# Kernel optimization log

Measured on AMD Instinct MI355X. Metric: run time of the kernel, lower is better.

## Reference

```python
import jax, jax.numpy as jnp
import numpy as np

B, C, H, W, K, O, KS = 32, 16, 256, 256, 4, 16, 3
C4 = C // 4


def setup_inputs() -> dict:
    key = jax.random.key(0)
    ks = jax.random.split(key, 6)
    return {
        "x": jax.random.normal(ks[0], (B, C, H, W), dtype=jnp.float32),
        "weight": jax.random.normal(ks[1], (K, O, C, KS, KS), dtype=jnp.float32),
        "attn_w1": jax.random.normal(ks[2], (C4, C), dtype=jnp.float32) * 0.1,
        "attn_b1": jnp.zeros((C4,), dtype=jnp.float32),
        "attn_w2": jax.random.normal(ks[3], (K, C4), dtype=jnp.float32) * 0.1,
        "attn_b2": jnp.zeros((K,), dtype=jnp.float32),
    }


def reference(x, weight, attn_w1, attn_b1, attn_w2, attn_b2):
    # Attention branch: global avg pool -> 1x1 conv -> relu -> 1x1 conv -> softmax over K
    pooled = x.mean(axis=(2, 3))                                  # (B, C)
    h = jax.nn.relu(pooled @ attn_w1.T + attn_b1)                 # (B, C//4)
    attn = jax.nn.softmax(h @ attn_w2.T + attn_b2, axis=1)        # (B, K)

    # Per-sample aggregated kernel: sum_k attn[b,k] * weight[k]
    agg_w = jnp.einsum('bk,koihw->boihw', attn, weight)           # (B, O, C, KS, KS)

    # Per-sample conv2d (equivalent to torch grouped conv with groups=B)
    pad = ((1, 1), (1, 1))
    def per_sample(xi, wi):
        # xi: (C, H, W), wi: (O, C, KS, KS)
        return jax.lax.conv_general_dilated(
            xi[None], wi, window_strides=(1, 1), padding=pad,
            dimension_numbers=('NCHW', 'OIHW', 'NCHW'))[0]
    return jax.vmap(per_sample)(x, agg_w)                         # (B, O, H, W)
```

## Files before the change

kernel.cpp:

```cpp
#include <hip/hip_runtime.h>

#define BD  32
#define CD  16
#define HD  256
#define WD  256
#define KD  4
#define OD  16
#define C4D 4

typedef __attribute__((ext_vector_type(8))) short short8v;
typedef __attribute__((ext_vector_type(4))) float float4v;

__device__ float          g_partial[2048];
__device__ unsigned short g_wfrag[BD * 2 * 5 * 64 * 8];

__device__ __forceinline__ unsigned short bf16_rne(float f) {
    unsigned u = __builtin_bit_cast(unsigned, f);
    u += 0x7FFFu + ((u >> 16) & 1u);
    return (unsigned short)(u >> 16);
}
__device__ __forceinline__ float bf16_to_f(unsigned short h) {
    unsigned u = ((unsigned)h) << 16;
    return __builtin_bit_cast(float, u);
}

__global__ void pool_kernel(const float* __restrict__ x) {
    const int plane = blockIdx.x >> 2;
    const int part  = blockIdx.x & 3;
    const float4* xp4 = reinterpret_cast<const float4*>(
        x + (size_t)plane * (HD * WD) + part * (HD * WD / 4));

    float4 v[16];
    #pragma unroll
    for (int i = 0; i < 16; ++i) v[i] = xp4[threadIdx.x + i * 256];
    float s = 0.f;
    #pragma unroll
    for (int i = 0; i < 16; ++i) s += (v[i].x + v[i].y) + (v[i].z + v[i].w);

    __shared__ float red[256];
    red[threadIdx.x] = s;
    __syncthreads();
    for (int off = 128; off > 0; off >>= 1) {
        if (threadIdx.x < off) red[threadIdx.x] += red[threadIdx.x + off];
        __syncthreads();
    }
    if (threadIdx.x == 0) g_partial[blockIdx.x] = red[0];
}

__global__ void attn_agg_kernel(const float* __restrict__ w1, const float* __restrict__ b1,
                                const float* __restrict__ w2, const float* __restrict__ b2,
                                const float* __restrict__ weight) {
    const int b = blockIdx.x;

    float p[CD];
    #pragma unroll
    for (int c = 0; c < CD; ++c) {
        const int i0 = (b * CD + c) * 4;
        p[c] = (g_partial[i0] + g_partial[i0 + 1] + g_partial[i0 + 2] + g_partial[i0 + 3])
               * (1.f / (HD * WD));
    }

    float h[C4D];
    #pragma unroll
    for (int j = 0; j < C4D; ++j) {
        float s = b1[j];
        #pragma unroll
        for (int c = 0; c < CD; ++c) s = fmaf(p[c], w1[j * CD + c], s);
        h[j] = fmaxf(s, 0.f);
    }

    float lg[KD];
    float mx = -1e30f;
    #pragma unroll
    for (int k = 0; k < KD; ++k) {
        float s = b2[k];
        #pragma unroll
        for (int j = 0; j < C4D; ++j) s = fmaf(h[j], w2[k * C4D + j], s);
        lg[k] = s;
        mx = fmaxf(mx, s);
    }
    float se = 0.f;
    #pragma unroll
    for (int k = 0; k < KD; ++k) { lg[k] = expf(lg[k] - mx); se += lg[k]; }
    const float inv = 1.f / se;
    float at[KD];
    #pragma unroll
    for (int k = 0; k < KD; ++k) at[k] = lg[k] * inv;

    for (int e = threadIdx.x; e < 5120; e += 256) {
        const int prod = e / 2560;
        const int rem  = e % 2560;
        const int s    = rem / 512;
        const int lr   = rem % 512;
        const int lane = lr >> 3;
        const int i    = lr & 7;
        const int o    = lane & 15;
        const int kg   = lane >> 4;
        const int kk   = kg * 8 + i;
        const int tl   = kk >> 4;
        const int c    = kk & 15;
        const int tap  = 2 * s + tl;
        float v = 0.f;
        if (tap < 9) {
            #pragma unroll
            for (int k = 0; k < KD; ++k)
                v = fmaf(at[k], weight[((k * OD + o) * CD + c) * 9 + tap], v);
        }
        const unsigned short hi = bf16_rne(v);
        unsigned short val = hi;
        if (prod == 1) val = bf16_rne(v - bf16_to_f(hi));
        g_wfrag[b * 5120 + e] = val;
    }
}

__global__ __launch_bounds__(256, 2)
void conv_kernel(const float* __restrict__ x, float* __restrict__ out) {
    const int b  = blockIdx.y;
    const int tx = blockIdx.x & 3;
    const int ty = blockIdx.x >> 2;
    const int x0 = tx * 64, y0 = ty * 16;

    __shared__ unsigned short xs[18 * 66 * 24];

    for (int e = threadIdx.x; e < 18 * 66; e += 256) {
        const int r   = e / 66;
        const int col = e - r * 66;
        const int gy  = y0 - 1 + r;
        const int gx  = x0 - 1 + col;
        const bool ok = (gy >= 0) && (gy < HD) && (gx >= 0) && (gx < WD);
        const float* px = x + ((size_t)b * CD * HD * WD) + (size_t)gy * WD + gx;
        unsigned d[8];
        #pragma unroll
        for (int j = 0; j < 8; ++j) {
            float v0 = 0.f, v1 = 0.f;
            if (ok) {
                v0 = px[(size_t)(2 * j)     * (HD * WD)];
                v1 = px[(size_t)(2 * j + 1) * (HD * WD)];
            }
            d[j] = (unsigned)bf16_rne(v0) | ((unsigned)bf16_rne(v1) << 16);
        }
        unsigned* dst = reinterpret_cast<unsigned*>(&xs[e * 24]);
        *reinterpret_cast<uint4*>(dst)     = make_uint4(d[0], d[1], d[2], d[3]);
        *reinterpret_cast<uint4*>(dst + 4) = make_uint4(d[4], d[5], d[6], d[7]);
    }

    const int lane = threadIdx.x & 63;
    const int wv   = threadIdx.x >> 6;

    short8v whi[5], wlo[5];
    {
        const unsigned short* wf = g_wfrag + b * 5120;
        #pragma unroll
        for (int s = 0; s < 5; ++s) {
            whi[s] = *(const short8v*)&wf[s * 512 + lane * 8];
            wlo[s] = *(const short8v*)&wf[2560 + s * 512 + lane * 8];
        }
    }

    const int m     = lane & 15;
    const int kg    = lane >> 4;
    const int tl    = kg >> 1;
    const int chalf = kg & 1;
    int aoff[5];
    #pragma unroll
    for (int s = 0; s < 5; ++s) {
        int tap = 2 * s + tl;
        if (tap > 8) tap = 8;
        const int dy = tap / 3 - 1, dx = tap % 3 - 1;
        aoff[s] = (dy * 66 + dx) * 24;
    }
    const int colbase = 1 + 16 * wv + m;

    __syncthreads();

    #pragma unroll 1
    for (int q2 = 0; q2 < 8; ++q2) {
        const int qa = 2 * q2;
        const int pa = ((qa + 1) * 66 + colbase) * 24 + chalf * 8;
        const int pb = pa + 66 * 24;
        float4v acca = {0.f, 0.f, 0.f, 0.f};
        float4v accb = {0.f, 0.f, 0.f, 0.f};
        #pragma unroll
        for (int s = 0; s < 5; ++s) {
            const short8v Aa = *(const short8v*)&xs[pa + aoff[s]];
            const short8v Ab = *(const short8v*)&xs[pb + aoff[s]];
            acca = __builtin_amdgcn_mfma_f32_16x16x32_bf16(Aa, whi[s], acca, 0, 0, 0);
            accb = __builtin_amdgcn_mfma_f32_16x16x32_bf16(Ab, whi[s], accb, 0, 0, 0);
            acca = __builtin_amdgcn_mfma_f32_16x16x32_bf16(Aa, wlo[s], acca, 0, 0, 0);
            accb = __builtin_amdgcn_mfma_f32_16x16x32_bf16(Ab, wlo[s], accb, 0, 0, 0);
        }
        const int o  = lane & 15;
        const int xc = x0 + 16 * wv + kg * 4;
        float4 va = make_float4(acca[0], acca[1], acca[2], acca[3]);
        float4 vb = make_float4(accb[0], accb[1], accb[2], accb[3]);
        *reinterpret_cast<float4*>(
            &out[((size_t)(b * OD + o) * HD + (y0 + qa)) * WD + xc]) = va;
        *reinterpret_cast<float4*>(
            &out[((size_t)(b * OD + o) * HD + (y0 + qa + 1)) * WD + xc]) = vb;
    }
}

extern "C" void kernel_launch(void* const* d_in, const int* in_sizes, int n_in,
                              void* d_out, int out_size, void* d_ws, size_t ws_size,
                              hipStream_t stream) {
    (void)in_sizes; (void)n_in; (void)out_size; (void)d_ws; (void)ws_size;
    const float* x      = (const float*)d_in[0];
    const float* weight = (const float*)d_in[1];
    const float* w1     = (const float*)d_in[2];
    const float* b1     = (const float*)d_in[3];
    const float* w2     = (const float*)d_in[4];
    const float* b2     = (const float*)d_in[5];
    float* out = (float*)d_out;

    pool_kernel<<<2048, 256, 0, stream>>>(x);
    attn_agg_kernel<<<32, 256, 0, stream>>>(w1, b1, w2, b2, weight);
    conv_kernel<<<dim3(64, 32), 256, 0, stream>>>(x, out);
}
```

Baseline: 299.8 us.

## Emit bf16 copy of input during pooling and load it in conv

The pooling pass now also writes a bf16 copy of the whole input to a global scratch buffer. The conv kernel stages its halo tile from that buffer with wide 8-byte row loads plus a small edge-column path, instead of scalar fp32 gathers converted per element. The attention/aggregation kernel is split across four blocks per sample for more parallelism. This adds a 64 MB bf16 write and read in exchange for halving conv input bytes and coalescing the tile load.

```diff
diff --git a/kernel.cpp b/kernel.cpp
--- a/kernel.cpp
+++ b/kernel.cpp
@@ -12,6 +12,7 @@
 typedef __attribute__((ext_vector_type(4))) float float4v;
 
 __device__ float          g_partial[2048];
+__device__ unsigned short g_xbf[(size_t)BD * CD * HD * WD];
 __device__ unsigned short g_wfrag[BD * 2 * 5 * 64 * 8];
 
 __device__ __forceinline__ unsigned short bf16_rne(float f) {
@@ -27,15 +28,22 @@
 __global__ void pool_kernel(const float* __restrict__ x) {
     const int plane = blockIdx.x >> 2;
     const int part  = blockIdx.x & 3;
-    const float4* xp4 = reinterpret_cast<const float4*>(
-        x + (size_t)plane * (HD * WD) + part * (HD * WD / 4));
+    const size_t base = (size_t)plane * (HD * WD) + part * (HD * WD / 4);
+    const float4* xp4 = reinterpret_cast<const float4*>(x + base);
 
     float4 v[16];
     #pragma unroll
     for (int i = 0; i < 16; ++i) v[i] = xp4[threadIdx.x + i * 256];
+
     float s = 0.f;
     #pragma unroll
-    for (int i = 0; i < 16; ++i) s += (v[i].x + v[i].y) + (v[i].z + v[i].w);
+    for (int i = 0; i < 16; ++i) {
+        s += (v[i].x + v[i].y) + (v[i].z + v[i].w);
+        ushort4 h;
+        h.x = bf16_rne(v[i].x); h.y = bf16_rne(v[i].y);
+        h.z = bf16_rne(v[i].z); h.w = bf16_rne(v[i].w);
+        *reinterpret_cast<ushort4*>(&g_xbf[base + (size_t)(threadIdx.x + i * 256) * 4]) = h;
+    }
 
     __shared__ float red[256];
     red[threadIdx.x] = s;
@@ -50,7 +58,8 @@
 __global__ void attn_agg_kernel(const float* __restrict__ w1, const float* __restrict__ b1,
                                 const float* __restrict__ w2, const float* __restrict__ b2,
                                 const float* __restrict__ weight) {
-    const int b = blockIdx.x;
+    const int b  = blockIdx.x >> 2;
+    const int e0 = (blockIdx.x & 3) * 1280;
 
     float p[CD];
     #pragma unroll
@@ -87,7 +96,7 @@
     #pragma unroll
     for (int k = 0; k < KD; ++k) at[k] = lg[k] * inv;
 
-    for (int e = threadIdx.x; e < 5120; e += 256) {
+    for (int e = e0 + threadIdx.x; e < e0 + 1280; e += 256) {
         const int prod = e / 2560;
         const int rem  = e % 2560;
         const int s    = rem / 512;
@@ -114,7 +123,7 @@
 }
 
 __global__ __launch_bounds__(256, 2)
-void conv_kernel(const float* __restrict__ x, float* __restrict__ out) {
+void conv_kernel(float* __restrict__ out) {
     const int b  = blockIdx.y;
     const int tx = blockIdx.x & 3;
     const int ty = blockIdx.x >> 2;
@@ -122,23 +131,53 @@
 
     __shared__ unsigned short xs[18 * 66 * 24];
 
-    for (int e = threadIdx.x; e < 18 * 66; e += 256) {
-        const int r   = e / 66;
-        const int col = e - r * 66;
+    for (int grp = threadIdx.x; grp < 288; grp += 256) {
+        const int r  = grp >> 4;
+        const int j  = grp & 15;
+        const int gy = y0 - 1 + r;
+        const int gx = x0 + 4 * j;
+        const bool ok = (gy >= 0) && (gy < HD);
+        uint2 v[16];
+        #pragma unroll
+        for (int c = 0; c < 16; ++c) {
+            v[c] = make_uint2(0u, 0u);
+            if (ok)
+                v[c] = *reinterpret_cast<const uint2*>(
+                    &g_xbf[((size_t)(b * CD + c) * HD + gy) * WD + gx]);
+        }
+        #pragma unroll
+        for (int p = 0; p < 4; ++p) {
+            unsigned d[8];
+            #pragma unroll
+            for (int i = 0; i < 8; ++i) {
+                const unsigned a0 = (p < 2) ? v[2 * i].x     : v[2 * i].y;
+                const unsigned a1 = (p < 2) ? v[2 * i + 1].x : v[2 * i + 1].y;
+                d[i] = (p & 1) ? ((a0 >> 16) | (a1 & 0xFFFF0000u))
+                               : ((a0 & 0xFFFFu) | (a1 << 16));
+            }
+            const int e = r * 66 + 4 * j + 1 + p;
+            unsigned* dst = reinterpret_cast<unsigned*>(&xs[e * 24]);
+            *reinterpret_cast<uint4*>(dst)     = make_uint4(d[0], d[1], d[2], d[3]);
+            *reinterpret_cast<uint4*>(dst + 4) = make_uint4(d[4], d[5], d[6], d[7]);
+        }
+    }
+    if (threadIdx.x < 36) {
+        const int r   = threadIdx.x >> 1;
+        const int col = (threadIdx.x & 1) ? 65 : 0;
         const int gy  = y0 - 1 + r;
         const int gx  = x0 - 1 + col;
         const bool ok = (gy >= 0) && (gy < HD) && (gx >= 0) && (gx < WD);
-        const float* px = x + ((size_t)b * CD * HD * WD) + (size_t)gy * WD + gx;
         unsigned d[8];
         #pragma unroll
-        for (int j = 0; j < 8; ++j) {
-            float v0 = 0.f, v1 = 0.f;
+        for (int i = 0; i < 8; ++i) {
+            unsigned u0 = 0, u1 = 0;
             if (ok) {
-                v0 = px[(size_t)(2 * j)     * (HD * WD)];
-                v1 = px[(size_t)(2 * j + 1) * (HD * WD)];
+                u0 = g_xbf[((size_t)(b * CD + 2 * i)     * HD + gy) * WD + gx];
+                u1 = g_xbf[((size_t)(b * CD + 2 * i + 1) * HD + gy) * WD + gx];
             }
-            d[j] = (unsigned)bf16_rne(v0) | ((unsigned)bf16_rne(v1) << 16);
-        }
+            d[i] = u0 | (u1 << 16);
+        }
+        const int e = r * 66 + col;
         unsigned* dst = reinterpret_cast<unsigned*>(&xs[e * 24]);
         *reinterpret_cast<uint4*>(dst)     = make_uint4(d[0], d[1], d[2], d[3]);
         *reinterpret_cast<uint4*>(dst + 4) = make_uint4(d[4], d[5], d[6], d[7]);
@@ -213,6 +252,6 @@
     float* out = (float*)d_out;
 
     pool_kernel<<<2048, 256, 0, stream>>>(x);
-    attn_agg_kernel<<<32, 256, 0, stream>>>(w1, b1, w2, b2, weight);
-    conv_kernel<<<dim3(64, 32), 256, 0, stream>>>(x, out);
-}
+    attn_agg_kernel<<<128, 256, 0, stream>>>(w1, b1, w2, b2, weight);
+    conv_kernel<<<dim3(64, 32), 256, 0, stream>>>(out);
+}
```

Result: no change. 297.5 us (-0.8%).

## Pre-convert input to padded bf16 interleaved layout in pool pass, read directly in conv

Applied to the files above, without the earlier changes.

The pooling kernel now also writes a zero-padded, channel-interleaved bf16 copy of x to a global buffer while it sums. The conv kernel then drops its shared-memory staging and fp32-to-bf16 conversion and loads MFMA operands straight from that buffer through the caches. Pooling partials are reorganised per stripe, the weight aggregation is spread over more blocks, and conv occupancy is raised. This trades an extra global write and read of the bf16 copy, plus cache-dependent halo reuse, for removing the LDS fill and a second fp32 pass over x.

```diff
diff --git a/kernel.cpp b/kernel.cpp
--- a/kernel.cpp
+++ b/kernel.cpp
@@ -11,7 +11,8 @@
 typedef __attribute__((ext_vector_type(8))) short short8v;
 typedef __attribute__((ext_vector_type(4))) float float4v;
 
-__device__ float          g_partial[2048];
+__device__ float          g_partial[64 * 16 * 8];
+__device__ unsigned short g_xi[(size_t)64 * 258 * 258 * 8];
 __device__ unsigned short g_wfrag[BD * 2 * 5 * 64 * 8];
 
 __device__ __forceinline__ unsigned short bf16_rne(float f) {
@@ -24,40 +25,69 @@
     return __builtin_bit_cast(float, u);
 }
 
-__global__ void pool_kernel(const float* __restrict__ x) {
-    const int plane = blockIdx.x >> 2;
-    const int part  = blockIdx.x & 3;
-    const float4* xp4 = reinterpret_cast<const float4*>(
-        x + (size_t)plane * (HD * WD) + part * (HD * WD / 4));
-
-    float4 v[16];
-    #pragma unroll
-    for (int i = 0; i < 16; ++i) v[i] = xp4[threadIdx.x + i * 256];
-    float s = 0.f;
-    #pragma unroll
-    for (int i = 0; i < 16; ++i) s += (v[i].x + v[i].y) + (v[i].z + v[i].w);
-
-    __shared__ float red[256];
-    red[threadIdx.x] = s;
+__global__ __launch_bounds__(256)
+void pool_kernel(const float* __restrict__ x) {
+    const int bb     = blockIdx.x >> 4;
+    const int stripe = blockIdx.x & 15;
+    const int b      = bb >> 1;
+    const int chalf  = bb & 1;
+    const int tid    = threadIdx.x;
+
+    float s8[8] = {0.f, 0.f, 0.f, 0.f, 0.f, 0.f, 0.f, 0.f};
+
+    #pragma unroll 2
+    for (int i = 0; i < 16; ++i) {
+        const int y = stripe * 16 + i;
+        const size_t prow = (size_t)y * WD + tid;
+        float f[8];
+        #pragma unroll
+        for (int ci = 0; ci < 8; ++ci) {
+            f[ci] = x[(size_t)(b * CD + chalf * 8 + ci) * (HD * WD) + prow];
+            s8[ci] += f[ci];
+        }
+        const unsigned d0 = (unsigned)bf16_rne(f[0]) | ((unsigned)bf16_rne(f[1]) << 16);
+        const unsigned d1 = (unsigned)bf16_rne(f[2]) | ((unsigned)bf16_rne(f[3]) << 16);
+        const unsigned d2 = (unsigned)bf16_rne(f[4]) | ((unsigned)bf16_rne(f[5]) << 16);
+        const unsigned d3 = (unsigned)bf16_rne(f[6]) | ((unsigned)bf16_rne(f[7]) << 16);
+        *reinterpret_cast<uint4*>(
+            &g_xi[(((size_t)bb * 258 + (y + 1)) * 258 + (tid + 1)) * 8]) =
+            make_uint4(d0, d1, d2, d3);
+    }
+
+    #pragma unroll
+    for (int ci = 0; ci < 8; ++ci) {
+        float v = s8[ci];
+        #pragma unroll
+        for (int off = 32; off > 0; off >>= 1) v += __shfl_down(v, off, 64);
+        s8[ci] = v;
+    }
+    __shared__ float ws[4][8];
+    const int lane = tid & 63, wv = tid >> 6;
+    if (lane == 0) {
+        #pragma unroll
+        for (int ci = 0; ci < 8; ++ci) ws[wv][ci] = s8[ci];
+    }
     __syncthreads();
-    for (int off = 128; off > 0; off >>= 1) {
-        if (threadIdx.x < off) red[threadIdx.x] += red[threadIdx.x + off];
-        __syncthreads();
-    }
-    if (threadIdx.x == 0) g_partial[blockIdx.x] = red[0];
+    if (tid < 8)
+        g_partial[(bb * 16 + stripe) * 8 + tid] =
+            ws[0][tid] + ws[1][tid] + ws[2][tid] + ws[3][tid];
 }
 
 __global__ void attn_agg_kernel(const float* __restrict__ w1, const float* __restrict__ b1,
                                 const float* __restrict__ w2, const float* __restrict__ b2,
                                 const float* __restrict__ weight) {
-    const int b = blockIdx.x;
+    const int b  = blockIdx.x >> 2;
+    const int e0 = (blockIdx.x & 3) * 1280;
 
     float p[CD];
     #pragma unroll
     for (int c = 0; c < CD; ++c) {
-        const int i0 = (b * CD + c) * 4;
-        p[c] = (g_partial[i0] + g_partial[i0 + 1] + g_partial[i0 + 2] + g_partial[i0 + 3])
-               * (1.f / (HD * WD));
+        const int bb = b * 2 + (c >> 3);
+        const int ci = c & 7;
+        float s = 0.f;
+        #pragma unroll
+        for (int st = 0; st < 16; ++st) s += g_partial[(bb * 16 + st) * 8 + ci];
+        p[c] = s * (1.f / (HD * WD));
     }
 
     float h[C4D];
@@ -87,7 +117,7 @@
     #pragma unroll
     for (int k = 0; k < KD; ++k) at[k] = lg[k] * inv;
 
-    for (int e = threadIdx.x; e < 5120; e += 256) {
+    for (int e = e0 + threadIdx.x; e < e0 + 1280; e += 256) {
         const int prod = e / 2560;
         const int rem  = e % 2560;
         const int s    = rem / 512;
@@ -113,37 +143,12 @@
     }
 }
 
-__global__ __launch_bounds__(256, 2)
-void conv_kernel(const float* __restrict__ x, float* __restrict__ out) {
+__global__ __launch_bounds__(256, 4)
+void conv_kernel(float* __restrict__ out) {
     const int b  = blockIdx.y;
     const int tx = blockIdx.x & 3;
     const int ty = blockIdx.x >> 2;
     const int x0 = tx * 64, y0 = ty * 16;
-
-    __shared__ unsigned short xs[18 * 66 * 24];
-
-    for (int e = threadIdx.x; e < 18 * 66; e += 256) {
-        const int r   = e / 66;
-        const int col = e - r * 66;
-        const int gy  = y0 - 1 + r;
-        const int gx  = x0 - 1 + col;
-        const bool ok = (gy >= 0) && (gy < HD) && (gx >= 0) && (gx < WD);
-        const float* px = x + ((size_t)b * CD * HD * WD) + (size_t)gy * WD + gx;
-        unsigned d[8];
-        #pragma unroll
-        for (int j = 0; j < 8; ++j) {
-            float v0 = 0.f, v1 = 0.f;
-            if (ok) {
-                v0 = px[(size_t)(2 * j)     * (HD * WD)];
-                v1 = px[(size_t)(2 * j + 1) * (HD * WD)];
-            }
-            d[j] = (unsigned)bf16_rne(v0) | ((unsigned)bf16_rne(v1) << 16);
-        }
-        unsigned* dst = reinterpret_cast<unsigned*>(&xs[e * 24]);
-        *reinterpret_cast<uint4*>(dst)     = make_uint4(d[0], d[1], d[2], d[3]);
-        *reinterpret_cast<uint4*>(dst + 4) = make_uint4(d[4], d[5], d[6], d[7]);
-    }
-
     const int lane = threadIdx.x & 63;
     const int wv   = threadIdx.x >> 6;
 
@@ -161,42 +166,46 @@
     const int kg    = lane >> 4;
     const int tl    = kg >> 1;
     const int chalf = kg & 1;
+    const int bb    = b * 2 + chalf;
+    const int col   = x0 + wv * 16 + m;
+    const unsigned short* bptr =
+        g_xi + (((size_t)bb * 258 + (y0 + 1)) * 258 + (col + 1)) * 8;
+
     int aoff[5];
     #pragma unroll
     for (int s = 0; s < 5; ++s) {
         int tap = 2 * s + tl;
         if (tap > 8) tap = 8;
         const int dy = tap / 3 - 1, dx = tap % 3 - 1;
-        aoff[s] = (dy * 66 + dx) * 24;
-    }
-    const int colbase = 1 + 16 * wv + m;
-
-    __syncthreads();
+        aoff[s] = (dy * 258 + dx) * 8;
+    }
+
+    const int o  = lane & 15;
+    const int xc = x0 + wv * 16 + kg * 4;
 
     #pragma unroll 1
     for (int q2 = 0; q2 < 8; ++q2) {
         const int qa = 2 * q2;
-        const int pa = ((qa + 1) * 66 + colbase) * 24 + chalf * 8;
-        const int pb = pa + 66 * 24;
+        const unsigned short* pa = bptr + qa * (258 * 8);
+        const unsigned short* pb = pa + 258 * 8;
         float4v acca = {0.f, 0.f, 0.f, 0.f};
         float4v accb = {0.f, 0.f, 0.f, 0.f};
         #pragma unroll
         for (int s = 0; s < 5; ++s) {
-            const short8v Aa = *(const short8v*)&xs[pa + aoff[s]];
-            const short8v Ab = *(const short8v*)&xs[pb + aoff[s]];
+            const short8v Aa = *(const short8v*)(pa + aoff[s]);
+            const short8v Ab = *(const short8v*)(pb + aoff[s]);
             acca = __builtin_amdgcn_mfma_f32_16x16x32_bf16(Aa, whi[s], acca, 0, 0, 0);
             accb = __builtin_amdgcn_mfma_f32_16x16x32_bf16(Ab, whi[s], accb, 0, 0, 0);
             acca = __builtin_amdgcn_mfma_f32_16x16x32_bf16(Aa, wlo[s], acca, 0, 0, 0);
             accb = __builtin_amdgcn_mfma_f32_16x16x32_bf16(Ab, wlo[s], accb, 0, 0, 0);
         }
-        const int o  = lane & 15;
-        const int xc = x0 + 16 * wv + kg * 4;
+        const int y = y0 + qa;
         float4 va = make_float4(acca[0], acca[1], acca[2], acca[3]);
         float4 vb = make_float4(accb[0], accb[1], accb[2], accb[3]);
         *reinterpret_cast<float4*>(
-            &out[((size_t)(b * OD + o) * HD + (y0 + qa)) * WD + xc]) = va;
+            &out[((size_t)(b * OD + o) * HD + y) * WD + xc]) = va;
         *reinterpret_cast<float4*>(
-            &out[((size_t)(b * OD + o) * HD + (y0 + qa + 1)) * WD + xc]) = vb;
+            &out[((size_t)(b * OD + o) * HD + (y + 1)) * WD + xc]) = vb;
     }
 }
 
@@ -212,7 +221,7 @@
     const float* b2     = (const float*)d_in[5];
     float* out = (float*)d_out;
 
-    pool_kernel<<<2048, 256, 0, stream>>>(x);
-    attn_agg_kernel<<<32, 256, 0, stream>>>(w1, b1, w2, b2, weight);
-    conv_kernel<<<dim3(64, 32), 256, 0, stream>>>(x, out);
-}
+    pool_kernel<<<1024, 256, 0, stream>>>(x);
+    attn_agg_kernel<<<128, 256, 0, stream>>>(w1, b1, w2, b2, weight);
+    conv_kernel<<<dim3(64, 32), 256, 0, stream>>>(out);
+}
```

Result: slower. 311.4 us (+3.9%).
